# Kernel optimization log

Hardware: AMD Instinct MI355X
Metric: run time of the kernel (lower is better)

## Reference

```python
import jax, jax.numpy as jnp
import numpy as np

KERNEL = (7, 7)
NUM_CH = 4
EPS = 1e-06
ROPE_BASE = 10000.0


def _rel_dist():
    coords = [np.arange(k, dtype=np.float32) - k // 2 for k in KERNEL]
    g = np.meshgrid(*coords, indexing='ij')
    d = np.sqrt(sum(gi ** 2 for gi in g))
    return jnp.asarray(d.reshape(-1)), float(d.max())


def silu(x):
    return x * jax.nn.sigmoid(x)


def rmsnorm(x, w):
    rms = jnp.sqrt(jnp.mean(x * x, axis=-1, keepdims=True) + EPS)
    return x / rms * w


def apply_rope(x):
    # x: (B, L, H, D); positions run over dim -2 (matches torch default)
    H, D = x.shape[-2], x.shape[-1]
    half = D // 2
    pos = jnp.arange(H, dtype=jnp.float32)
    freqs = 1.0 / (ROPE_BASE ** (jnp.arange(half, dtype=x.dtype) / half))
    ang = pos[:, None] * freqs  # (H, half)
    cos, sin = jnp.cos(ang), jnp.sin(ang)
    x1, x2 = x[..., :half], x[..., half:2 * half]
    return jnp.concatenate([x1 * cos - x2 * sin, x1 * sin + x2 * cos], axis=-1)


def unfold2d(x):
    # x: (B, Hs, Ws, C) -> (B, Hs, Ws, k1*k2, C), row-major kernel order
    B, Hs, Ws, C = x.shape
    k1, k2 = KERNEL
    xp = jnp.pad(x, ((0, 0), ((k1 - 1) // 2, k1 // 2), ((k2 - 1) // 2, k2 // 2), (0, 0)))
    wins = [xp[:, i:i + Hs, j:j + Ws, :] for i in range(k1) for j in range(k2)]
    return jnp.stack(wins, axis=3)


def setup_inputs() -> dict:
    key = jax.random.key(0)
    ks = jax.random.split(key, 8)
    C = 256
    x = jax.random.normal(ks[0], (2, 64, 64, C), dtype=jnp.float32)
    W_qkv = jax.random.normal(ks[1], (C, 3 * C), dtype=jnp.float32) * 0.02
    w_qnorm = jnp.ones((C // NUM_CH,), dtype=jnp.float32)
    w_knorm = jnp.ones((C // NUM_CH,), dtype=jnp.float32)
    W_wp = jax.random.normal(ks[2], (C, 2 * NUM_CH), dtype=jnp.float32) * 0.02
    b_wp = jax.random.normal(ks[3], (2 * NUM_CH,), dtype=jnp.float32) * 0.02
    w_onorm = jnp.ones((C,), dtype=jnp.float32)
    W_out = jax.random.normal(ks[4], (C, C), dtype=jnp.float32) * 0.02
    W_gate = jax.random.normal(ks[5], (C, C), dtype=jnp.float32) * 0.02
    b_gate = 2.0 * jnp.ones((C,), dtype=jnp.float32)
    return {"x": x, "W_qkv": W_qkv, "w_qnorm": w_qnorm, "w_knorm": w_knorm,
            "W_wp": W_wp, "b_wp": b_wp, "w_onorm": w_onorm, "W_out": W_out,
            "W_gate": W_gate, "b_gate": b_gate}


def reference(x, W_qkv, w_qnorm, w_knorm, W_wp, b_wp, w_onorm, W_out, W_gate, b_gate):
    rel_dist, max_dist = _rel_dist()
    B, Hs, Ws, C = x.shape
    L = Hs * Ws
    H = NUM_CH
    D = C // H
    Wsz = KERNEL[0] * KERNEL[1]
    scale = D ** (-0.5)

    qkv = silu(x @ W_qkv)
    q, k, v = jnp.split(qkv, 3, axis=-1)

    q_flat = apply_rope(rmsnorm(q.reshape(B, L, H, D), w_qnorm))
    k_flat = apply_rope(rmsnorm(k.reshape(B, L, H, D), w_knorm))
    k = k_flat.reshape(B, Hs, Ws, C)

    wp = silu(x @ W_wp + b_wp)  # (B, Hs, Ws, 2H)
    width_raw, sharp_raw = jnp.split(wp, 2, axis=-1)
    width = jax.nn.sigmoid(width_raw) * max_dist + 0.5
    sharpness = jax.nn.sigmoid(sharp_raw) * 9.5 + 0.5

    k_win = unfold2d(k).reshape(B, L, Wsz, H, D)
    v_win = unfold2d(v).reshape(B, L, Wsz, H, D)

    scores = jnp.einsum('blhd,blwhd->blhw', q_flat, k_win) * scale
    width_f = width.reshape(B, L, H, 1)
    sharp_f = sharpness.reshape(B, L, H, 1)
    soft_mask = jax.nn.sigmoid((width_f - rel_dist) * sharp_f)
    scores = scores - (1.0 - soft_mask) * 10000.0
    attn = jax.nn.softmax(scores, axis=-1)

    out = jnp.einsum('blhw,blwhd->blhd', attn, v_win).reshape(B, Hs, Ws, C)
    out = rmsnorm(out, w_onorm)

    gate = jax.nn.sigmoid(silu(v @ W_gate + b_gate))
    merged = gate * v + (1.0 - gate) * out
    return silu(merged @ W_out)
```

## Files before the change

kernel.cpp:

```cpp
#include <hip/hip_runtime.h>
#include <hip/hip_fp16.h>
#include <math.h>

__device__ __forceinline__ float sigm(float x)  { return 1.0f / (1.0f + __expf(-x)); }
__device__ __forceinline__ float siluf(float x) { return x * sigm(x); }

typedef _Float16 half8  __attribute__((ext_vector_type(8)));
typedef _Float16 half4  __attribute__((ext_vector_type(4)));
typedef float    f32x4  __attribute__((ext_vector_type(4)));
typedef unsigned u32x2  __attribute__((ext_vector_type(2)));

__device__ __forceinline__ void gld16(const void* g, void* l) {
    __builtin_amdgcn_global_load_lds(
        (const __attribute__((address_space(1))) unsigned*)g,
        (__attribute__((address_space(3))) unsigned*)l, 16, 0, 0);
}

template <int N>
__device__ __forceinline__ void wait_vmcnt() {
    if constexpr (N == 0)      asm volatile("s_waitcnt vmcnt(0)" ::: "memory");
    else if constexpr (N == 3) asm volatile("s_waitcnt vmcnt(3)" ::: "memory");
    else if constexpr (N == 5) asm volatile("s_waitcnt vmcnt(5)" ::: "memory");
    else if constexpr (N == 6) asm volatile("s_waitcnt vmcnt(6)" ::: "memory");
}

template <int MI, int AMODE>
__device__ __forceinline__ void gemm_core16(
    const __half* __restrict__ A16,
    const __half* __restrict__ Bhi, const __half* __restrict__ Blo,
    int nbs, int m0, int n0, int t, int koff, f32x4 (&acc)[MI][4])
{
    __shared__ short As[2][MI * 1024], BsHi[2][4096], BsLo[2][4096];
    const int lane = t & 63, wave = t >> 6;
    const int wm = (wave >> 1) * (MI << 4), wn = (wave & 1) << 6;
    const int fr = lane & 15, fq = lane >> 4;
    constexpr int NL = MI / 2 + 4;

    auto stage = [&](int kb, int buf) {
        const int kc = (kb + koff) & 7;
#pragma unroll
        for (int hf = 0; hf < MI / 2; ++hf) {
            const int rr = wave * (MI << 3) + (hf << 4);
            size_t ga;
            if (AMODE == 0)
                ga = (((size_t)(kc * 8192 + m0 + rr)) << 5) + (lane << 3);
            else
                ga = (((size_t)(m0 + rr + (lane >> 2))) << 8) + (kc << 5) + ((lane & 3) << 3);
            gld16(A16 + ga, &As[buf][rr << 5]);
        }
#pragma unroll
        for (int hf = 0; hf < 2; ++hf) {
            const int rr = (wave << 5) + (hf << 4);
            const size_t gb = (((size_t)(kc * nbs + n0 + rr)) << 5) + (lane << 3);
            gld16(Bhi + gb, &BsHi[buf][rr << 5]);
            gld16(Blo + gb, &BsLo[buf][rr << 5]);
        }
    };

    stage(0, 0);
#pragma unroll
    for (int kb = 0; kb < 8; ++kb) {
        const int cur = kb & 1;
        if (kb < 7) {
            stage(kb + 1, cur ^ 1);
            wait_vmcnt<NL>();
        } else {
            wait_vmcnt<0>();
        }
        __builtin_amdgcn_s_barrier();

        half8 a[MI], bh[4], bl[4];
#pragma unroll
        for (int i = 0; i < MI; ++i)
            a[i] = *(const half8*)&As[cur][((wm + (i << 4) + fr) << 5) + (fq << 3)];
#pragma unroll
        for (int i = 0; i < 4; ++i) {
            const int boff = ((wn + (i << 4) + fr) << 5) + (fq << 3);
            bh[i] = *(const half8*)&BsHi[cur][boff];
            bl[i] = *(const half8*)&BsLo[cur][boff];
        }
#pragma unroll
        for (int mi = 0; mi < MI; ++mi)
#pragma unroll
            for (int ni = 0; ni < 4; ++ni) {
                acc[mi][ni] = __builtin_amdgcn_mfma_f32_16x16x32_f16(a[mi], bh[ni], acc[mi][ni], 0, 0, 0);
                acc[mi][ni] = __builtin_amdgcn_mfma_f32_16x16x32_f16(a[mi], bl[ni], acc[mi][ni], 0, 0, 0);
            }

        if (kb < 7) __builtin_amdgcn_s_barrier();
    }
}

__device__ __forceinline__ void gemm_core64(
    const __half* __restrict__ A16,
    const __half* __restrict__ Bhi, const __half* __restrict__ Blo,
    int m0, int n0, int t, int koff, f32x4 (&acc)[4])
{
    __shared__ short As[2][2048], BsHi[2][2048], BsLo[2][2048];
    const int lane = t & 63, wave = t >> 6;
    const int wm = wave << 4;
    const int fr = lane & 15, fq = lane >> 4;

    auto stage = [&](int kb, int buf) {
        const int kc = (kb + koff) & 7;
        const int rr = wave << 4;
        const size_t ga = (((size_t)(m0 + rr + (lane >> 2))) << 8) + (kc << 5) + ((lane & 3) << 3);
        gld16(A16 + ga, &As[buf][rr << 5]);
        const size_t gb = (((size_t)(kc * 256 + n0 + rr)) << 5) + (lane << 3);
        gld16(Bhi + gb, &BsHi[buf][rr << 5]);
        gld16(Blo + gb, &BsLo[buf][rr << 5]);
    };

    stage(0, 0);
#pragma unroll
    for (int kb = 0; kb < 8; ++kb) {
        const int cur = kb & 1;
        if (kb < 7) {
            stage(kb + 1, cur ^ 1);
            wait_vmcnt<3>();
        } else {
            wait_vmcnt<0>();
        }
        __builtin_amdgcn_s_barrier();

        half8 a = *(const half8*)&As[cur][((wm + fr) << 5) + (fq << 3)];
        half8 bh[4], bl[4];
#pragma unroll
        for (int ni = 0; ni < 4; ++ni) {
            const int boff = (((ni << 4) + fr) << 5) + (fq << 3);
            bh[ni] = *(const half8*)&BsHi[cur][boff];
            bl[ni] = *(const half8*)&BsLo[cur][boff];
        }
#pragma unroll
        for (int ni = 0; ni < 4; ++ni) {
            acc[ni] = __builtin_amdgcn_mfma_f32_16x16x32_f16(a, bh[ni], acc[ni], 0, 0, 0);
            acc[ni] = __builtin_amdgcn_mfma_f32_16x16x32_f16(a, bl[ni], acc[ni], 0, 0, 0);
        }

        if (kb < 7) __builtin_amdgcn_s_barrier();
    }
}

__global__ __launch_bounds__(256) void prep_kernel(
    const float* __restrict__ x, const float* __restrict__ Wqkv,
    const float* __restrict__ Wgate, const float* __restrict__ Wout,
    const float* __restrict__ Wwp, const float* __restrict__ bwp,
    __half* __restrict__ xh,
    __half* __restrict__ wqh, __half* __restrict__ wql,
    __half* __restrict__ wgh, __half* __restrict__ wgl,
    __half* __restrict__ woh, __half* __restrict__ wol,
    float* __restrict__ width, float* __restrict__ sharp)
{
    __shared__ float xs[32][260];
    const int t = threadIdx.x;
    const int blk = blockIdx.x;
    if (blk < 256) {
        const int row0 = blk << 5;
        for (int e = t; e < 2048; e += 256) {
            int r = e >> 6, cc = (e & 63) << 2;
            *(float4*)&xs[r][cc] = *(const float4*)&x[(size_t)(row0 + r) * 256 + cc];
        }
        __syncthreads();
        const int r = t & 31, kb = t >> 5;
        __half hibuf[32];
#pragma unroll
        for (int i = 0; i < 32; ++i)
            hibuf[i] = __float2half(xs[r][(kb << 5) + i]);
        const size_t ob = ((size_t)(kb * 8192 + row0 + r)) << 5;
#pragma unroll
        for (int i = 0; i < 4; ++i)
            *(int4*)&xh[ob + (i << 3)] = *(int4*)&hibuf[i << 3];
        float a0 = 0.f, a1 = 0.f, a2 = 0.f, a3 = 0.f;
#pragma unroll 4
        for (int k = 0; k < 256; k += 4) {
            a0 += xs[r][k + 0] * Wwp[(k + 0) * 8 + kb];
            a1 += xs[r][k + 1] * Wwp[(k + 1) * 8 + kb];
            a2 += xs[r][k + 2] * Wwp[(k + 2) * 8 + kb];
            a3 += xs[r][k + 3] * Wwp[(k + 3) * 8 + kb];
        }
        const float acc = (a0 + a1) + (a2 + a3);
        float s = sigm(siluf(acc + bwp[kb]));
        const int row = row0 + r;
        if (kb < 4) width[row * 4 + kb] = s * 4.242640687119285f + 0.5f;
        else        sharp[row * 4 + kb - 4] = s * 9.5f + 0.5f;
    } else {
        const float* W; __half *Whi, *Wlo; int N, nb0, ncnt;
        if (blk < 288)      { W = Wqkv;  Whi = wqh; Wlo = wql; N = 768; nb0 = (blk - 256) * 24; ncnt = 24; }
        else if (blk < 296) { W = Wgate; Whi = wgh; Wlo = wgl; N = 256; nb0 = (blk - 288) * 32; ncnt = 32; }
        else                { W = Wout;  Whi = woh; Wlo = wol; N = 256; nb0 = (blk - 296) * 32; ncnt = 32; }
        for (int j = 0; j < ncnt; ++j)
            xs[j][t] = W[(size_t)t * N + nb0 + j];
        __syncthreads();
        for (int c = t; c < ncnt * 8; c += 256) {
            const int j = c >> 3, kb = c & 7;
            __half hibuf[32], lobuf[32];
#pragma unroll
            for (int i = 0; i < 32; ++i) {
                float v = xs[j][(kb << 5) + i];
                __half hv = __float2half(v);
                hibuf[i] = hv;
                lobuf[i] = __float2half(v - __half2float(hv));
            }
            const size_t ob = ((size_t)(kb * N + nb0 + j)) << 5;
#pragma unroll
            for (int i = 0; i < 4; ++i) {
                *(int4*)&Whi[ob + (i << 3)] = *(int4*)&hibuf[i << 3];
                *(int4*)&Wlo[ob + (i << 3)] = *(int4*)&lobuf[i << 3];
            }
        }
    }
}

__global__ __launch_bounds__(256, 3) void gemm_qkv(
    const __half* __restrict__ xh,
    const __half* __restrict__ wqh, const __half* __restrict__ wql,
    const float* __restrict__ wq, const float* __restrict__ wk,
    __half* __restrict__ qh, __half* __restrict__ kh, __half* __restrict__ vh)
{
    const int t  = threadIdx.x;
    const int m0 = blockIdx.y << 6, n0 = blockIdx.x << 7;
    f32x4 acc[2][4] = {};
    gemm_core16<2, 0>(xh, wqh, wql, 768, m0, n0, t, blockIdx.y & 7, acc);

    const int lane = t & 63, wave = t >> 6;
    const int wm = (wave >> 1) << 5, wn = (wave & 1) << 6;
    const int fr = lane & 15, fq = lane >> 4;
    const int gc0 = n0 + wn;
    const int seg = gc0 >> 8;
    const int h   = (gc0 >> 6) & 3;
    const int hc0 = h << 6;

#pragma unroll
    for (int mi = 0; mi < 2; ++mi)
#pragma unroll
        for (int ni = 0; ni < 4; ++ni)
#pragma unroll
            for (int r = 0; r < 4; ++r)
                acc[mi][ni][r] = siluf(acc[mi][ni][r]);

    if (seg == 2) {
#pragma unroll
        for (int mi = 0; mi < 2; ++mi)
#pragma unroll
            for (int r = 0; r < 4; ++r) {
                const size_t row = m0 + wm + (mi << 4) + (fq << 2) + r;
#pragma unroll
                for (int ni = 0; ni < 4; ++ni)
                    vh[row * 256 + hc0 + (ni << 4) + fr] = __float2half(acc[mi][ni][r]);
            }
    } else {
        const float* wnorm = seg ? wk : wq;
        float wv[4];
#pragma unroll
        for (int ni = 0; ni < 4; ++ni) wv[ni] = wnorm[(ni << 4) + fr];
        float cs[2], sn[2];
#pragma unroll
        for (int j = 0; j < 2; ++j) {
            const int d = (j << 4) + fr;
            const float freq = powf(10000.f, -(float)d * (1.f / 32.f));
            const float ang = (float)h * freq;
            cs[j] = cosf(ang); sn[j] = sinf(ang);
        }
        __half* dstbase = (seg ? kh : qh);
#pragma unroll
        for (int mi = 0; mi < 2; ++mi)
#pragma unroll
            for (int r = 0; r < 4; ++r) {
                float ss = acc[mi][0][r] * acc[mi][0][r] + acc[mi][1][r] * acc[mi][1][r]
                         + acc[mi][2][r] * acc[mi][2][r] + acc[mi][3][r] * acc[mi][3][r];
                ss += __shfl_xor(ss, 1); ss += __shfl_xor(ss, 2);
                ss += __shfl_xor(ss, 4); ss += __shfl_xor(ss, 8);
                const float rinv = 1.f / sqrtf(ss * (1.f / 64.f) + 1e-6f);
                float xv[4];
#pragma unroll
                for (int ni = 0; ni < 4; ++ni) xv[ni] = acc[mi][ni][r] * rinv * wv[ni];
                const float o0 = xv[0] * cs[0] - xv[2] * sn[0];
                const float o2 = xv[0] * sn[0] + xv[2] * cs[0];
                const float o1 = xv[1] * cs[1] - xv[3] * sn[1];
                const float o3 = xv[1] * sn[1] + xv[3] * cs[1];
                const size_t row = m0 + wm + (mi << 4) + (fq << 2) + r;
                __half* dst = dstbase + row * 256 + hc0;
                dst[fr]      = __float2half(o0);
                dst[16 + fr] = __float2half(o1);
                dst[32 + fr] = __float2half(o2);
                dst[48 + fr] = __float2half(o3);
            }
    }
}

__global__ __launch_bounds__(256, 2) void gemm_gate(
    const __half* __restrict__ vh,
    const __half* __restrict__ wgh, const __half* __restrict__ wgl,
    const float* __restrict__ bias, const float* __restrict__ attn_o,
    const float* __restrict__ sumsq4, const float* __restrict__ w_onorm,
    __half* __restrict__ mh)
{
    const int t  = threadIdx.x;
    const int m0 = blockIdx.y << 6, n0 = blockIdx.x << 6;
    f32x4 acc[4] = {};
    gemm_core64(vh, wgh, wgl, m0, n0, t, blockIdx.y & 7, acc);

    const int lane = t & 63, wave = t >> 6;
    const int wm = wave << 4;
    const int fr = lane & 15, fq = lane >> 4;

    float rmsf[4];
#pragma unroll
    for (int r = 0; r < 4; ++r) {
        const int m = m0 + wm + (fq << 2) + r;
        float4 s4 = *(const float4*)&sumsq4[(size_t)m * 4];
        rmsf[r] = 1.f / sqrtf((s4.x + s4.y + s4.z + s4.w) * (1.f / 256.f) + 1e-6f);
    }

#pragma unroll
    for (int ni = 0; ni < 4; ++ni) {
        const int n  = n0 + (ni << 4) + fr;
        const int mb = m0 + wm + (fq << 2);
        const float bb  = bias[n];
        const float won = w_onorm[n];
#pragma unroll
        for (int r = 0; r < 4; ++r) {
            const int m = mb + r;
            const float g  = sigm(siluf(acc[ni][r] + bb));
            const float vv = __half2float(vh[(size_t)m * 256 + n]);
            const float oo = attn_o[(size_t)m * 256 + n] * rmsf[r] * won;
            mh[(size_t)m * 256 + n] = __float2half(g * vv + (1.f - g) * oo);
        }
    }
}

__global__ __launch_bounds__(256, 2) void gemm_out(
    const __half* __restrict__ mh,
    const __half* __restrict__ woh, const __half* __restrict__ wol,
    float* __restrict__ out)
{
    const int t  = threadIdx.x;
    const int m0 = blockIdx.y << 6, n0 = blockIdx.x << 6;
    f32x4 acc[4] = {};
    gemm_core64(mh, woh, wol, m0, n0, t, blockIdx.y & 7, acc);

    const int lane = t & 63, wave = t >> 6;
    const int wm = wave << 4;
    const int fr = lane & 15, fq = lane >> 4;
#pragma unroll
    for (int ni = 0; ni < 4; ++ni) {
        const int n  = n0 + (ni << 4) + fr;
        const int mb = m0 + wm + (fq << 2);
#pragma unroll
        for (int r = 0; r < 4; ++r)
            out[(size_t)(mb + r) * 256 + n] = siluf(acc[ni][r]);
    }
}

#define PT 216

__global__ __launch_bounds__(256, 2) void attn_mfma(
    const __half* __restrict__ qh, const __half* __restrict__ kh,
    const __half* __restrict__ vh, const float* __restrict__ width,
    const float* __restrict__ sharp, float* __restrict__ attn_o,
    float* __restrict__ sumsq4)
{
    __shared__ short smem[27648];
    short* Ksh = smem;
    short* Psh = smem;
    short* Vt  = smem + 13824;

    const int t = threadIdx.x;
    const int lane = t & 63, wave = t >> 6;
    const int fr = lane & 15, fq = lane >> 4;
    const int patch = blockIdx.x, h = blockIdx.y, b = blockIdx.z;
    const int pr0 = (patch >> 3) << 3, pc0 = (patch & 7) << 3;
    const int t0 = (wave * 28) >> 4;

    float wd[4], sh[4]; int lq[4];
#pragma unroll
    for (int r = 0; r < 4; ++r) {
        const int q = (wave << 4) + (fq << 2) + r;
        lq[r] = (pr0 + (q >> 3)) * 64 + pc0 + (q & 7);
        wd[r] = width[((b << 12) + lq[r]) * 4 + h];
        sh[r] = sharp[((b << 12) + lq[r]) * 4 + h];
    }

    const int qrow = (wave << 4) + fr;
    const int lqr = (pr0 + (qrow >> 3)) * 64 + pc0 + (qrow & 7);
    const __half* qptr = qh + (((size_t)(b << 12) + lqr) << 8) + (h << 6) + (fq << 3);
    half8 a0 = *(const half8*)qptr;
    half8 a1 = *(const half8*)(qptr + 32);

    const int srow = t >> 4;
    const int d4 = (t & 15) << 2;
    const size_t cbase = (((size_t)b << 12) * 256) + (size_t)h * 64 + d4;

    u32x2 kb2[13], vb2[13];
#pragma unroll
    for (int p = 0; p < 13; ++p) {
        const int prow = (p << 4) + srow;
        const int pi = prow / 14, pj = prow - pi * 14;
        const int gr = pr0 - 3 + pi, gc = pc0 - 3 + pj;
        const bool ok = (prow < 196) & ((unsigned)gr < 64u) & ((unsigned)gc < 64u);
        const int grc = min(max(gr, 0), 63), gcc = min(max(gc, 0), 63);
        const size_t off = cbase + (size_t)(grc * 64 + gcc) * 256;
        u32x2 kv = *(const u32x2*)(kh + off);
        u32x2 vv = *(const u32x2*)(vh + off);
        const u32x2 z = {0u, 0u};
        kb2[p] = ok ? kv : z;
        vb2[p] = ok ? vv : z;
    }

    const int chunk = d4 >> 3, dlo = d4 & 7;
#pragma unroll
    for (int p = 0; p < 13; ++p) {
        const int prow = (p << 4) + srow;
        *(u32x2*)&Ksh[(prow << 6) + ((chunk ^ (prow & 7)) << 3) + dlo] = kb2[p];
        Vt[(d4)     * PT + prow] = (short)(vb2[p].x & 0xffffu);
        Vt[(d4 + 1) * PT + prow] = (short)(vb2[p].x >> 16);
        Vt[(d4 + 2) * PT + prow] = (short)(vb2[p].y & 0xffffu);
        Vt[(d4 + 3) * PT + prow] = (short)(vb2[p].y >> 16);
    }
    __syncthreads();

    f32x4 sc[8];
#pragma unroll
    for (int tl = 0; tl < 8; ++tl) {
        const int kr = ((t0 + tl) << 4) + fr;
        half8 b0 = *(const half8*)&Ksh[(kr << 6) + (((0 + fq) ^ (kr & 7)) << 3)];
        half8 b1 = *(const half8*)&Ksh[(kr << 6) + (((4 + fq) ^ (kr & 7)) << 3)];
        f32x4 z = {0.f, 0.f, 0.f, 0.f};
        z = __builtin_amdgcn_mfma_f32_16x16x32_f16(a0, b0, z, 0, 0, 0);
        sc[tl] = __builtin_amdgcn_mfma_f32_16x16x32_f16(a1, b1, z, 0, 0, 0);
    }

    float mx[4] = {-3e38f, -3e38f, -3e38f, -3e38f};
#pragma unroll
    for (int tl = 0; tl < 8; ++tl) {
        const int p = ((t0 + tl) << 4) + fr;
        const int pi = p / 14, pj = p - pi * 14;
        const bool pvld = p < 196;
#pragma unroll
        for (int r = 0; r < 4; ++r) {
            const int q = (wave << 4) + (fq << 2) + r;
            const int di = pi - 3 - ((q >> 3) & 7), dj = pj - 3 - (q & 7);
            const bool win = pvld & ((unsigned)(di + 3) <= 6u) & ((unsigned)(dj + 3) <= 6u);
            const float rel = sqrtf((float)(di * di + dj * dj));
            const float mk = sigm((wd[r] - rel) * sh[r]);
            float s = sc[tl][r] * 0.125f - (1.f - mk) * 10000.f;
            s = win ? s : -3e38f;
            sc[tl][r] = s;
            mx[r] = fmaxf(mx[r], s);
        }
    }
#pragma unroll
    for (int r = 0; r < 4; ++r) {
        mx[r] = fmaxf(mx[r], __shfl_xor(mx[r], 1));
        mx[r] = fmaxf(mx[r], __shfl_xor(mx[r], 2));
        mx[r] = fmaxf(mx[r], __shfl_xor(mx[r], 4));
        mx[r] = fmaxf(mx[r], __shfl_xor(mx[r], 8));
    }
    float sm[4] = {0.f, 0.f, 0.f, 0.f};
#pragma unroll
    for (int tl = 0; tl < 8; ++tl)
#pragma unroll
        for (int r = 0; r < 4; ++r) {
            const float e = __expf(sc[tl][r] - mx[r]);
            sc[tl][r] = e; sm[r] += e;
        }
#pragma unroll
    for (int r = 0; r < 4; ++r) {
        sm[r] += __shfl_xor(sm[r], 1);
        sm[r] += __shfl_xor(sm[r], 2);
        sm[r] += __shfl_xor(sm[r], 4);
        sm[r] += __shfl_xor(sm[r], 8);
        sm[r] = 1.f / sm[r];
    }

    __syncthreads();
#pragma unroll
    for (int tl = 0; tl < 8; ++tl)
#pragma unroll
        for (int r = 0; r < 4; ++r) {
            __half pv = __float2half(sc[tl][r] * sm[r]);
            Psh[((wave << 4) + (fq << 2) + r) * PT + ((t0 + tl) << 4) + fr] = *(short*)&pv;
        }
    asm volatile("s_waitcnt lgkmcnt(0)" ::: "memory");
    __builtin_amdgcn_sched_barrier(0);

    f32x4 o[4] = {};
    const int pra = (wave << 4) + fr;
    const int cb = t0 << 4;
#pragma unroll
    for (int s = 0; s < 4; ++s) {
        half8 pa = *(const half8*)&Psh[pra * PT + cb + (fq << 3) + (s << 5)];
#pragma unroll
        for (int dt = 0; dt < 4; ++dt) {
            half8 vbf = *(const half8*)&Vt[((dt << 4) + fr) * PT + cb + (fq << 3) + (s << 5)];
            o[dt] = __builtin_amdgcn_mfma_f32_16x16x32_f16(pa, vbf, o[dt], 0, 0, 0);
        }
    }

#pragma unroll
    for (int r = 0; r < 4; ++r) {
        float ss = o[0][r]*o[0][r] + o[1][r]*o[1][r] + o[2][r]*o[2][r] + o[3][r]*o[3][r];
        ss += __shfl_xor(ss, 1); ss += __shfl_xor(ss, 2);
        ss += __shfl_xor(ss, 4); ss += __shfl_xor(ss, 8);
        const size_t rowb = (((size_t)(b << 12) + lq[r]) << 8) + h * 64;
#pragma unroll
        for (int dt = 0; dt < 4; ++dt)
            attn_o[rowb + (dt << 4) + fr] = o[dt][r];
        if (fr == 0) sumsq4[(((b << 12) + lq[r]) << 2) + h] = ss;
    }
}

extern "C" void kernel_launch(void* const* d_in, const int* in_sizes, int n_in,
                              void* d_out, int out_size, void* d_ws, size_t ws_size,
                              hipStream_t stream)
{
    const float* x      = (const float*)d_in[0];
    const float* W_qkv  = (const float*)d_in[1];
    const float* w_qn   = (const float*)d_in[2];
    const float* w_kn   = (const float*)d_in[3];
    const float* W_wp   = (const float*)d_in[4];
    const float* b_wp   = (const float*)d_in[5];
    const float* w_on   = (const float*)d_in[6];
    const float* W_out  = (const float*)d_in[7];
    const float* W_gate = (const float*)d_in[8];
    const float* b_gate = (const float*)d_in[9];
    float* out = (float*)d_out;

    __half* ws16 = (__half*)d_ws;
    __half* xh  = ws16;
    __half* wqh = xh  + 2097152;
    __half* wql = wqh + 196608;
    __half* wgh = wql + 196608;
    __half* wgl = wgh + 65536;
    __half* woh = wgl + 65536;
    __half* wol = woh + 65536;
    __half* qhp = wol + 65536;
    __half* khp = qhp + 2097152;
    __half* vhp = khp + 2097152;
    __half* mh  = vhp + 2097152;
    float* attn_o = (float*)(mh + 2097152);
    float* widthp = attn_o + 2097152;
    float* sharpp = widthp + 32768;
    float* sumsq4 = sharpp + 32768;

    prep_kernel<<<304, 256, 0, stream>>>(x, W_qkv, W_gate, W_out, W_wp, b_wp,
                                         xh, wqh, wql, wgh, wgl, woh, wol,
                                         widthp, sharpp);
    gemm_qkv<<<dim3(6, 128), 256, 0, stream>>>(xh, wqh, wql, w_qn, w_kn,
                                               qhp, khp, vhp);
    attn_mfma<<<dim3(64, 4, 2), 256, 0, stream>>>(qhp, khp, vhp, widthp, sharpp,
                                                  attn_o, sumsq4);
    gemm_gate<<<dim3(4, 128), 256, 0, stream>>>(vhp, wgh, wgl, b_gate,
                                                attn_o, sumsq4, w_on, mh);
    gemm_out<<<dim3(4, 128), 256, 0, stream>>>(mh, woh, wol, out);
}
```

Measured before the change: 132.1 us.

## Merge gate and output GEMMs into one cooperative kernel with grid sync

Replaces the separate gate GEMM and output GEMM launches with a single cooperative kernel. A grid-wide sync sits between the phases so the merged activations are complete before the output GEMM reads them. Shared LDS staging is now passed in explicitly and reused by both phases. This removes one kernel launch and its gap, at the cost of a grid barrier, and it needs all 512 blocks to be co-resident.

```diff
diff --git a/kernel.cpp b/kernel.cpp
--- a/kernel.cpp
+++ b/kernel.cpp
@@ -1,6 +1,9 @@
 #include <hip/hip_runtime.h>
 #include <hip/hip_fp16.h>
+#include <hip/hip_cooperative_groups.h>
 #include <math.h>
+
+namespace cg = cooperative_groups;
 
 __device__ __forceinline__ float sigm(float x)  { return 1.0f / (1.0f + __expf(-x)); }
 __device__ __forceinline__ float siluf(float x) { return x * sigm(x); }
@@ -91,12 +94,15 @@
     }
 }
 
-__device__ __forceinline__ void gemm_core64(
+__device__ __forceinline__ void gemm_core64_lds(
+    short* lds,
     const __half* __restrict__ A16,
     const __half* __restrict__ Bhi, const __half* __restrict__ Blo,
     int m0, int n0, int t, int koff, f32x4 (&acc)[4])
 {
-    __shared__ short As[2][2048], BsHi[2][2048], BsLo[2][2048];
+    short* As   = lds;
+    short* BsHi = lds + 4096;
+    short* BsLo = lds + 8192;
     const int lane = t & 63, wave = t >> 6;
     const int wm = wave << 4;
     const int fr = lane & 15, fq = lane >> 4;
@@ -105,10 +111,10 @@
         const int kc = (kb + koff) & 7;
         const int rr = wave << 4;
         const size_t ga = (((size_t)(m0 + rr + (lane >> 2))) << 8) + (kc << 5) + ((lane & 3) << 3);
-        gld16(A16 + ga, &As[buf][rr << 5]);
+        gld16(A16 + ga, &As[buf * 2048 + (rr << 5)]);
         const size_t gb = (((size_t)(kc * 256 + n0 + rr)) << 5) + (lane << 3);
-        gld16(Bhi + gb, &BsHi[buf][rr << 5]);
-        gld16(Blo + gb, &BsLo[buf][rr << 5]);
+        gld16(Bhi + gb, &BsHi[buf * 2048 + (rr << 5)]);
+        gld16(Blo + gb, &BsLo[buf * 2048 + (rr << 5)]);
     };
 
     stage(0, 0);
@@ -123,13 +129,13 @@
         }
         __builtin_amdgcn_s_barrier();
 
-        half8 a = *(const half8*)&As[cur][((wm + fr) << 5) + (fq << 3)];
+        half8 a = *(const half8*)&As[cur * 2048 + ((wm + fr) << 5) + (fq << 3)];
         half8 bh[4], bl[4];
 #pragma unroll
         for (int ni = 0; ni < 4; ++ni) {
             const int boff = (((ni << 4) + fr) << 5) + (fq << 3);
-            bh[ni] = *(const half8*)&BsHi[cur][boff];
-            bl[ni] = *(const half8*)&BsLo[cur][boff];
+            bh[ni] = *(const half8*)&BsHi[cur * 2048 + boff];
+            bl[ni] = *(const half8*)&BsLo[cur * 2048 + boff];
         }
 #pragma unroll
         for (int ni = 0; ni < 4; ++ni) {
@@ -288,67 +294,66 @@
     }
 }
 
-__global__ __launch_bounds__(256, 2) void gemm_gate(
+__global__ __launch_bounds__(256, 2) void gemm_gateout(
     const __half* __restrict__ vh,
     const __half* __restrict__ wgh, const __half* __restrict__ wgl,
     const float* __restrict__ bias, const float* __restrict__ attn_o,
     const float* __restrict__ sumsq4, const float* __restrict__ w_onorm,
-    __half* __restrict__ mh)
-{
-    const int t  = threadIdx.x;
-    const int m0 = blockIdx.y << 6, n0 = blockIdx.x << 6;
-    f32x4 acc[4] = {};
-    gemm_core64(vh, wgh, wgl, m0, n0, t, blockIdx.y & 7, acc);
-
+    __half* __restrict__ mh,
+    const __half* __restrict__ woh, const __half* __restrict__ wol,
+    float* __restrict__ out)
+{
+    __shared__ short lds[12288];
+    const int t = threadIdx.x;
     const int lane = t & 63, wave = t >> 6;
     const int wm = wave << 4;
     const int fr = lane & 15, fq = lane >> 4;
-
-    float rmsf[4];
-#pragma unroll
-    for (int r = 0; r < 4; ++r) {
-        const int m = m0 + wm + (fq << 2) + r;
-        float4 s4 = *(const float4*)&sumsq4[(size_t)m * 4];
-        rmsf[r] = 1.f / sqrtf((s4.x + s4.y + s4.z + s4.w) * (1.f / 256.f) + 1e-6f);
-    }
-
-#pragma unroll
-    for (int ni = 0; ni < 4; ++ni) {
-        const int n  = n0 + (ni << 4) + fr;
-        const int mb = m0 + wm + (fq << 2);
-        const float bb  = bias[n];
-        const float won = w_onorm[n];
+    const int m0 = blockIdx.y << 6, n0 = blockIdx.x << 6;
+    const int koff = blockIdx.y & 7;
+
+    {
+        f32x4 acc[4] = {};
+        gemm_core64_lds(lds, vh, wgh, wgl, m0, n0, t, koff, acc);
+
+        float rmsf[4];
 #pragma unroll
         for (int r = 0; r < 4; ++r) {
-            const int m = mb + r;
-            const float g  = sigm(siluf(acc[ni][r] + bb));
-            const float vv = __half2float(vh[(size_t)m * 256 + n]);
-            const float oo = attn_o[(size_t)m * 256 + n] * rmsf[r] * won;
-            mh[(size_t)m * 256 + n] = __float2half(g * vv + (1.f - g) * oo);
-        }
-    }
-}
-
-__global__ __launch_bounds__(256, 2) void gemm_out(
-    const __half* __restrict__ mh,
-    const __half* __restrict__ woh, const __half* __restrict__ wol,
-    float* __restrict__ out)
-{
-    const int t  = threadIdx.x;
-    const int m0 = blockIdx.y << 6, n0 = blockIdx.x << 6;
-    f32x4 acc[4] = {};
-    gemm_core64(mh, woh, wol, m0, n0, t, blockIdx.y & 7, acc);
-
-    const int lane = t & 63, wave = t >> 6;
-    const int wm = wave << 4;
-    const int fr = lane & 15, fq = lane >> 4;
-#pragma unroll
-    for (int ni = 0; ni < 4; ++ni) {
-        const int n  = n0 + (ni << 4) + fr;
-        const int mb = m0 + wm + (fq << 2);
-#pragma unroll
-        for (int r = 0; r < 4; ++r)
-            out[(size_t)(mb + r) * 256 + n] = siluf(acc[ni][r]);
+            const int m = m0 + wm + (fq << 2) + r;
+            float4 s4 = *(const float4*)&sumsq4[(size_t)m * 4];
+            rmsf[r] = 1.f / sqrtf((s4.x + s4.y + s4.z + s4.w) * (1.f / 256.f) + 1e-6f);
+        }
+#pragma unroll
+        for (int ni = 0; ni < 4; ++ni) {
+            const int n  = n0 + (ni << 4) + fr;
+            const int mb = m0 + wm + (fq << 2);
+            const float bb  = bias[n];
+            const float won = w_onorm[n];
+#pragma unroll
+            for (int r = 0; r < 4; ++r) {
+                const int m = mb + r;
+                const float g  = sigm(siluf(acc[ni][r] + bb));
+                const float vv = __half2float(vh[(size_t)m * 256 + n]);
+                const float oo = attn_o[(size_t)m * 256 + n] * rmsf[r] * won;
+                mh[(size_t)m * 256 + n] = __float2half(g * vv + (1.f - g) * oo);
+            }
+        }
+    }
+
+    __threadfence();
+    cg::this_grid().sync();
+    __syncthreads();
+
+    {
+        f32x4 acc[4] = {};
+        gemm_core64_lds(lds, mh, woh, wol, m0, n0, t, koff, acc);
+#pragma unroll
+        for (int ni = 0; ni < 4; ++ni) {
+            const int n  = n0 + (ni << 4) + fr;
+            const int mb = m0 + wm + (fq << 2);
+#pragma unroll
+            for (int r = 0; r < 4; ++r)
+                out[(size_t)(mb + r) * 256 + n] = siluf(acc[ni][r]);
+        }
     }
 }
 
@@ -550,7 +555,19 @@
                                                qhp, khp, vhp);
     attn_mfma<<<dim3(64, 4, 2), 256, 0, stream>>>(qhp, khp, vhp, widthp, sharpp,
                                                   attn_o, sumsq4);
-    gemm_gate<<<dim3(4, 128), 256, 0, stream>>>(vhp, wgh, wgl, b_gate,
-                                                attn_o, sumsq4, w_on, mh);
-    gemm_out<<<dim3(4, 128), 256, 0, stream>>>(mh, woh, wol, out);
-}
+    {
+        const __half* vh_a = vhp;
+        const __half* wgh_a = wgh; const __half* wgl_a = wgl;
+        const float* bias_a = b_gate; const float* ao_a = attn_o;
+        const float* ss_a = sumsq4; const float* won_a = w_on;
+        __half* mh_a = mh;
+        const __half* woh_a = woh; const __half* wol_a = wol;
+        float* out_a = out;
+        void* args[] = {(void*)&vh_a, (void*)&wgh_a, (void*)&wgl_a,
+                        (void*)&bias_a, (void*)&ao_a, (void*)&ss_a,
+                        (void*)&won_a, (void*)&mh_a, (void*)&woh_a,
+                        (void*)&wol_a, (void*)&out_a};
+        hipLaunchCooperativeKernel((void*)gemm_gateout, dim3(4, 128),
+                                   dim3(256), args, 0, stream);
+    }
+}
```

Result: slower. 276.3 us (+109.2%).
